# Kernel optimization log

Measured on AMD Instinct MI355X. Metric: run time of the kernel, lower is better.

Reference implementation:

```python
import jax, jax.numpy as jnp
import numpy as np

B, N, D, C, S = 128, 100000, 256, 2000, 751  # batch, memory size, feat dim, num classes, source classes
TEMP = 0.05
EPS = 1e-06


def _l2norm(x):
    return x / jnp.linalg.norm(x, axis=-1, keepdims=True)


def setup_inputs() -> dict:
    key = jax.random.key(0)
    k1, k2, k3, k4, k5 = jax.random.split(key, 5)
    inputs = _l2norm(jax.random.normal(k1, (B, D), dtype=jnp.float32))
    inputs2 = _l2norm(jax.random.normal(k2, (B, D), dtype=jnp.float32))
    features = _l2norm(jax.random.normal(k3, (N, D), dtype=jnp.float32))
    labels = jax.random.randint(k4, (N,), 0, C)
    labels = labels.at[:C].set(jnp.arange(C))  # ensure labels.max()+1 == C
    indexes = jax.random.randint(k5, (B,), 0, N)
    return {"inputs": inputs, "inputs2": inputs2, "features": features,
            "labels": labels, "indexes": indexes, "source_classes": S}


def reference(inputs, inputs2, features, labels, indexes, source_classes):
    # memory-bank logits, [B, N]
    logits = (inputs @ features.T) / TEMP
    logits2 = (inputs2 @ features.T) / TEMP
    targets = labels[indexes]  # [B]

    # per-class counts and segment-mean of logits over the bank, [C, B]
    nums = jax.ops.segment_sum(jnp.ones((N,), jnp.float32), labels, num_segments=C)  # [C]
    denom = jnp.where(nums > 0, nums, 1.0)[:, None]  # [C, 1]
    sim = jax.ops.segment_sum(logits.T, labels, num_segments=C) / denom   # [C, B]
    sim2 = jax.ops.segment_sum(logits2.T, labels, num_segments=C) / denom  # [C, B]

    # MSE between class-probability maps over the first source_classes classes
    p1 = sim[:source_classes].T   # [B, S]
    p2 = sim2[:source_classes].T  # [B, S]
    diff = jax.nn.softmax(p1, axis=1) - jax.nn.softmax(p2, axis=1)
    loss_mse = jnp.sum(diff * diff) / source_classes

    # hard-positive/negative mining: per-class max of logits (0 for empty classes)
    seg_max = jax.ops.segment_max(logits.T, labels, num_segments=C)  # [C, B], -inf where empty
    present = (nums > 0)  # [C]
    sim_hard = jnp.where(present[:, None], seg_max, 0.0).T  # [B, C]
    # for the target class, use the hardest (min) positive instead
    seg_min = jax.ops.segment_min(logits.T, labels, num_segments=C)  # [C, B]
    b_idx = jnp.arange(B)
    sim_hard = sim_hard.at[b_idx, targets].set(seg_min[targets, b_idx])

    # masked softmax over present classes + NLL
    mask = present.astype(jnp.float32)[None, :]  # [1, C]
    exps = jnp.exp(sim_hard) * mask
    masked_sim = exps / (jnp.sum(exps, axis=1, keepdims=True) + EPS)
    loss_con = -jnp.mean(jnp.log(masked_sim[b_idx, targets] + EPS))

    return (loss_con, loss_mse)
```

## Files before the change

### kernel.cpp

```cpp
#include <hip/hip_runtime.h>
#include <hip/hip_bf16.h>

#define BB 128
#define NN 100000
#define DD 256
#define CC 2000
#define SS 751
#define INVTEMP 20.0f
#define EPSV 1e-6f

#define HIST_BLOCKS 391
#define PREP_BLOCKS 32
#define NTILES_MAX 3563

typedef __attribute__((ext_vector_type(8))) short bf16x8;
typedef __attribute__((ext_vector_type(8))) unsigned short u16x8;
typedef __attribute__((ext_vector_type(4))) float f32x4;

__device__ __forceinline__ unsigned short f2bf(float x) {
    unsigned int u = __float_as_uint(x);
    u += 0x7fffu + ((u >> 16) & 1u);
    return (unsigned short)(u >> 16);
}

__device__ __forceinline__ bf16x8 cvt8(float4 a, float4 b) {
    union { unsigned u[4]; bf16x8 v; } cv;
    asm("v_cvt_pk_bf16_f32 %0, %1, %2" : "=v"(cv.u[0]) : "v"(a.x), "v"(a.y));
    asm("v_cvt_pk_bf16_f32 %0, %1, %2" : "=v"(cv.u[1]) : "v"(a.z), "v"(a.w));
    asm("v_cvt_pk_bf16_f32 %0, %1, %2" : "=v"(cv.u[2]) : "v"(b.x), "v"(b.y));
    asm("v_cvt_pk_bf16_f32 %0, %1, %2" : "=v"(cv.u[3]) : "v"(b.z), "v"(b.w));
    return cv.v;
}

__global__ __launch_bounds__(256) void hist_prep_kernel(
    const int* __restrict__ labels, int* __restrict__ counts,
    const float* __restrict__ in1, const float* __restrict__ in2,
    unsigned short* __restrict__ inb)
{
    int bid = blockIdx.x;
    if (bid < HIST_BLOCKS) {
        int n = bid * 256 + threadIdx.x;
        if (n < NN) atomicAdd(&counts[labels[n]], 1);
    } else {
        int ch = (bid - HIST_BLOCKS) * 256 + threadIdx.x;
        if (ch >= 8192) return;
        int l  = ch & 63;
        int kc = (ch >> 6) & 7;
        int nr = ch >> 9;
        int row = nr * 16 + (l & 15);
        const float* src = (row < BB) ? (in1 + (size_t)row * DD)
                                      : (in2 + (size_t)(row - BB) * DD);
        int k0 = kc * 32 + ((l >> 4) << 3);
        u16x8 o;
        #pragma unroll
        for (int j = 0; j < 8; ++j) o[j] = f2bf(src[k0 + j]);
        *(u16x8*)(inb + (size_t)ch * 8) = o;
    }
}

__global__ __launch_bounds__(256) void scan_kernel(const int* __restrict__ counts,
                                                   int* __restrict__ tile_start,
                                                   int* __restrict__ cursor,
                                                   int* __restrict__ tile_meta,
                                                   int* __restrict__ ntiles_total,
                                                   float* __restrict__ out) {
    const int PT = 8;
    int tid = threadIdx.x;
    if (tid == 0) { out[0] = 0.f; out[1] = 0.f; }
    int tcnt[PT];
    int tot = 0;
    #pragma unroll
    for (int i = 0; i < PT; ++i) {
        int c = tid * PT + i;
        tcnt[i] = (c < CC) ? ((counts[c] + 63) >> 6) : 0;
        tot += tcnt[i];
    }
    __shared__ int sh[256];
    sh[tid] = tot;
    __syncthreads();
    for (int ofs = 1; ofs < 256; ofs <<= 1) {
        int v = (tid >= ofs) ? sh[tid - ofs] : 0;
        __syncthreads();
        sh[tid] += v;
        __syncthreads();
    }
    if (tid == 255) *ntiles_total = sh[255];
    int run = sh[tid] - tot;
    #pragma unroll
    for (int i = 0; i < PT; ++i) {
        int c = tid * PT + i;
        if (c < CC) {
            tile_start[c] = run;
            cursor[c] = run << 6;
            for (int j = 0; j < tcnt[i]; ++j)
                tile_meta[run + j] = (c << 5) | j;
        }
        run += tcnt[i];
    }
}

__global__ void scatter_idx(const int* __restrict__ labels, int* __restrict__ cursor,
                            int* __restrict__ sorted_idx) {
    int n = blockIdx.x * 256 + threadIdx.x;
    if (n < NN) {
        int c = labels[n];
        int p = atomicAdd(&cursor[c], 1);
        sorted_idx[p] = n;
    }
}

__global__ __launch_bounds__(512, 4) void mm_kernel(
    const float* __restrict__ features, const unsigned short* __restrict__ inb,
    const int* __restrict__ sorted_idx, const int* __restrict__ tile_meta,
    const int* __restrict__ counts, const int* __restrict__ ntiles_total,
    float* __restrict__ part_max, float* __restrict__ part_min,
    float* __restrict__ part_sA, float* __restrict__ part_sB)
{
    const int t = blockIdx.x;
    if (t >= *ntiles_total) return;
    const int tid = threadIdx.x;
    const int w   = tid >> 6;
    const int l   = tid & 63;
    const int meta = tile_meta[t];
    const int base_local = (meta & 31) << 6;
    const int cnt  = counts[meta >> 5];
    const int vrows = cnt - base_local;

    __shared__ __align__(16) char ldsF[65536];

    #pragma unroll
    for (int i2 = 0; i2 < 8; ++i2) {
        int row = w * 8 + i2;
        int idx = t * 64 + ((row < vrows) ? row : 0);
        int n   = sorted_idx[idx];
        const float* src = features + (size_t)n * DD + ((l ^ (row & 7)) << 2);
        __builtin_amdgcn_global_load_lds(
            (const __attribute__((address_space(1))) void*)src,
            (__attribute__((address_space(3))) void*)(&ldsF[0] + (row << 10)),
            16, 0, 0);
    }
    __syncthreads();

    f32x4 acc[4][2];
    #pragma unroll
    for (int ma = 0; ma < 4; ++ma)
        #pragma unroll
        for (int nb = 0; nb < 2; ++nb)
            acc[ma][nb] = (f32x4){0.f, 0.f, 0.f, 0.f};

    const int rlow = l & 15;
    const int cbase = (l >> 4) << 1;

    bf16x8 bcur0 = *(const bf16x8*)(inb + (((size_t)((2 * w + 0) * 8 + 0) * 64 + l) << 3));
    bf16x8 bcur1 = *(const bf16x8*)(inb + (((size_t)((2 * w + 1) * 8 + 0) * 64 + l) << 3));

    __builtin_amdgcn_s_setprio(1);
    #pragma unroll
    for (int kc = 0; kc < 8; ++kc) {
        bf16x8 bnx0 = bcur0, bnx1 = bcur1;
        if (kc < 7) {
            bnx0 = *(const bf16x8*)(inb + (((size_t)((2 * w + 0) * 8 + kc + 1) * 64 + l) << 3));
            bnx1 = *(const bf16x8*)(inb + (((size_t)((2 * w + 1) * 8 + kc + 1) * 64 + l) << 3));
        }
        #pragma unroll
        for (int ma = 0; ma < 4; ++ma) {
            int r  = 16 * ma + rlow;
            int x  = r & 7;
            int c0 = kc * 8 + cbase;
            const char* Lr = &ldsF[0] + (r << 10);
            float4 f0 = *(const float4*)(Lr + (((c0    ) ^ x) << 4));
            float4 f1 = *(const float4*)(Lr + (((c0 + 1) ^ x) << 4));
            bf16x8 a = cvt8(f0, f1);
            acc[ma][0] = __builtin_amdgcn_mfma_f32_16x16x32_bf16(a, bcur0, acc[ma][0], 0, 0, 0);
            acc[ma][1] = __builtin_amdgcn_mfma_f32_16x16x32_bf16(a, bcur1, acc[ma][1], 0, 0, 0);
        }
        bcur0 = bnx0; bcur1 = bnx1;
    }
    __builtin_amdgcn_s_setprio(0);

    const int h4 = (l >> 4) << 2;
    float sm[2] = {0.f, 0.f};
    float mx[2] = {-3.4e38f, -3.4e38f};
    float mn[2] = { 3.4e38f,  3.4e38f};
    #pragma unroll
    for (int ma = 0; ma < 4; ++ma) {
        #pragma unroll
        for (int reg = 0; reg < 4; ++reg) {
            bool valid = (16 * ma + h4 + reg) < vrows;
            if (valid) {
                #pragma unroll
                for (int nb = 0; nb < 2; ++nb) {
                    float v = acc[ma][nb][reg];
                    sm[nb] += v;
                    if (w < 4) {
                        mx[nb] = fmaxf(mx[nb], v);
                        mn[nb] = fminf(mn[nb], v);
                    }
                }
            }
        }
    }
    #pragma unroll
    for (int nb = 0; nb < 2; ++nb) {
        sm[nb] += __shfl_xor(sm[nb], 16);
        sm[nb] += __shfl_xor(sm[nb], 32);
        if (w < 4) {
            mx[nb] = fmaxf(mx[nb], __shfl_xor(mx[nb], 16));
            mx[nb] = fmaxf(mx[nb], __shfl_xor(mx[nb], 32));
            mn[nb] = fminf(mn[nb], __shfl_xor(mn[nb], 16));
            mn[nb] = fminf(mn[nb], __shfl_xor(mn[nb], 32));
        }
    }
    if (l < 16) {
        #pragma unroll
        for (int nb = 0; nb < 2; ++nb) {
            int col = 32 * (w & 3) + 16 * nb + l;
            size_t p = (size_t)t * 128 + col;
            if (w < 4) { part_max[p] = mx[nb]; part_min[p] = mn[nb]; part_sA[p] = sm[nb]; }
            else       { part_sB[p] = sm[nb]; }
        }
    }
}


__device__ __forceinline__ float blk_reduce_sum(float v) {
    __shared__ float sh[4];
    int lane = threadIdx.x & 63, w = threadIdx.x >> 6;
    #pragma unroll
    for (int o = 32; o; o >>= 1) v += __shfl_down(v, o, 64);
    __syncthreads();
    if (lane == 0) sh[w] = v;
    __syncthreads();
    return sh[0] + sh[1] + sh[2] + sh[3];
}

__device__ __forceinline__ float blk_reduce_max(float v) {
    __shared__ float sh[4];
    int lane = threadIdx.x & 63, w = threadIdx.x >> 6;
    #pragma unroll
    for (int o = 32; o; o >>= 1) v = fmaxf(v, __shfl_down(v, o, 64));
    __syncthreads();
    if (lane == 0) sh[w] = v;
    __syncthreads();
    return fmaxf(fmaxf(sh[0], sh[1]), fmaxf(sh[2], sh[3]));
}

__global__ __launch_bounds__(256) void finalize_kernel(
    const float* __restrict__ part_max, const float* __restrict__ part_min,
    const float* __restrict__ part_sA, const float* __restrict__ part_sB,
    const int* __restrict__ tile_start, const int* __restrict__ counts,
    const int* __restrict__ labels, const int* __restrict__ indexes,
    float* __restrict__ out)
{
    const int b   = blockIdx.x;
    const int tid = threadIdx.x;
    const int tgt = labels[indexes[b]];

    __shared__ float a1[SS], a2[SS];
    __shared__ float sh_etgt;

    float local = 0.f;
    for (int c = tid; c < CC; c += 256) {
        int cnt = counts[c];
        if (cnt > 0) {
            int t0 = tile_start[c];
            int nt = (cnt + 63) >> 6;
            bool src = (c < SS);
            float mx = -3.4e38f, sA = 0.f, sB = 0.f;
            for (int j = 0; j < nt; ++j) {
                size_t p = (size_t)(t0 + j) * 128 + b;
                mx = fmaxf(mx, part_max[p]);
                if (src) { sA += part_sA[p]; sB += part_sB[p]; }
            }
            float v = mx;
            if (c == tgt) {
                float mn = 3.4e38f;
                for (int j = 0; j < nt; ++j)
                    mn = fminf(mn, part_min[(size_t)(t0 + j) * 128 + b]);
                v = mn;
            }
            float e = expf(v * INVTEMP);
            local += e;
            if (c == tgt) sh_etgt = e;
            if (src) {
                float icnt = INVTEMP / (float)cnt;
                a1[c] = sA * icnt;
                a2[c] = sB * icnt;
            }
        } else if (c < SS) {
            a1[c] = 0.f;
            a2[c] = 0.f;
        }
    }
    float sum_e = blk_reduce_sum(local);
    float etgt = sh_etgt;
    float loss_con_b = -logf(etgt / (sum_e + EPSV) + EPSV);

    float m1 = -3.4e38f, m2 = -3.4e38f;
    for (int c = tid; c < SS; c += 256) { m1 = fmaxf(m1, a1[c]); m2 = fmaxf(m2, a2[c]); }
    m1 = blk_reduce_max(m1);
    m2 = blk_reduce_max(m2);
    float s1 = 0.f, s2 = 0.f;
    for (int c = tid; c < SS; c += 256) { s1 += expf(a1[c] - m1); s2 += expf(a2[c] - m2); }
    s1 = blk_reduce_sum(s1);
    s2 = blk_reduce_sum(s2);
    float inv1 = 1.f / s1, inv2 = 1.f / s2;
    float dsum = 0.f;
    for (int c = tid; c < SS; c += 256) {
        float d = expf(a1[c] - m1) * inv1 - expf(a2[c] - m2) * inv2;
        dsum += d * d;
    }
    dsum = blk_reduce_sum(dsum);
    if (tid == 0) {
        atomicAdd(&out[0], loss_con_b * (1.0f / (float)BB));
        atomicAdd(&out[1], dsum * (1.0f / (float)SS));
    }
}


extern "C" void kernel_launch(void* const* d_in, const int* in_sizes, int n_in,
                              void* d_out, int out_size, void* d_ws, size_t ws_size,
                              hipStream_t stream) {
    const float* inputs   = (const float*)d_in[0];
    const float* inputs2  = (const float*)d_in[1];
    const float* features = (const float*)d_in[2];
    const int*   labels   = (const int*)d_in[3];
    const int*   indexes  = (const int*)d_in[4];

    float* out = (float*)d_out;

    int* wsi = (int*)d_ws;
    int* counts     = wsi;
    int* tile_start = wsi + 2048;
    int* cursor     = wsi + 4096;
    int* ntiles     = wsi + 6144;
    unsigned short* inb = (unsigned short*)(wsi + 6160);
    int* tile_meta  = wsi + 38928;
    int* sorted_idx = wsi + 42496;
    float* part_max = (float*)(wsi + 270592);
    float* part_min = part_max + (size_t)NTILES_MAX * 128;
    float* part_sA  = part_min + (size_t)NTILES_MAX * 128;
    float* part_sB  = part_sA  + (size_t)NTILES_MAX * 128;

    hipMemsetAsync(counts, 0, 2048 * sizeof(int), stream);

    hist_prep_kernel<<<HIST_BLOCKS + PREP_BLOCKS, 256, 0, stream>>>(
        labels, counts, inputs, inputs2, inb);
    scan_kernel<<<1, 256, 0, stream>>>(counts, tile_start, cursor, tile_meta, ntiles, out);
    scatter_idx<<<HIST_BLOCKS, 256, 0, stream>>>(labels, cursor, sorted_idx);
    mm_kernel<<<NTILES_MAX, 512, 0, stream>>>(features, inb, sorted_idx, tile_meta,
                                              counts, ntiles,
                                              part_max, part_min, part_sA, part_sB);
    finalize_kernel<<<BB, 256, 0, stream>>>(part_max, part_min, part_sA, part_sB,
                                            tile_start, counts, labels, indexes, out);
}
```

Measured before the change: 98.91 us.

## Convert feature tile to bf16 once when staging into LDS

The feature tile is no longer copied into LDS as fp32 with async global_load_lds and then converted to bf16 by each of the 8 waves. Each thread now loads fp32 rows through registers, converts them to bf16 once, and writes them to a swizzled MFMA-ready LDS layout. This halves LDS use (32KB) and removes the redundant per-wave conversions and LDS reads. In exchange it loses the asynchronous direct-to-LDS load path, and the prefetch of the B operand across the k loop is dropped.

```diff
diff --git a/kernel.cpp b/kernel.cpp
--- a/kernel.cpp
+++ b/kernel.cpp
@@ -23,8 +23,8 @@
     return (unsigned short)(u >> 16);
 }
 
-__device__ __forceinline__ bf16x8 cvt8(float4 a, float4 b) {
-    union { unsigned u[4]; bf16x8 v; } cv;
+__device__ __forceinline__ u16x8 cvt8u(float4 a, float4 b) {
+    union { unsigned u[4]; u16x8 v; } cv;
     asm("v_cvt_pk_bf16_f32 %0, %1, %2" : "=v"(cv.u[0]) : "v"(a.x), "v"(a.y));
     asm("v_cvt_pk_bf16_f32 %0, %1, %2" : "=v"(cv.u[1]) : "v"(a.z), "v"(a.w));
     asm("v_cvt_pk_bf16_f32 %0, %1, %2" : "=v"(cv.u[2]) : "v"(b.x), "v"(b.y));
@@ -126,18 +126,27 @@
     const int cnt  = counts[meta >> 5];
     const int vrows = cnt - base_local;
 
-    __shared__ __align__(16) char ldsF[65536];
-
-    #pragma unroll
-    for (int i2 = 0; i2 < 8; ++i2) {
-        int row = w * 8 + i2;
-        int idx = t * 64 + ((row < vrows) ? row : 0);
+    __shared__ __align__(16) char ldsA[32768];
+
+    {
+        const int m0 = tid >> 3;
+        const int g  = tid & 7;
+        int idx = t * 64 + ((m0 < vrows) ? m0 : 0);
         int n   = sorted_idx[idx];
-        const float* src = features + (size_t)n * DD + ((l ^ (row & 7)) << 2);
-        __builtin_amdgcn_global_load_lds(
-            (const __attribute__((address_space(1))) void*)src,
-            (__attribute__((address_space(3))) void*)(&ldsF[0] + (row << 10)),
-            16, 0, 0);
+        const float* src = features + (size_t)n * DD;
+        const int ma = m0 >> 4;
+        #pragma unroll
+        for (int s = 0; s < 4; ++s) {
+            int k0 = s * 64 + g * 8;
+            float4 a = *(const float4*)(src + k0);
+            float4 b = *(const float4*)(src + k0 + 4);
+            u16x8 o = cvt8u(a, b);
+            int crow = s * 8 + g;
+            int kc   = crow >> 2;
+            int ks   = crow & 3;
+            int cch  = (ks << 4) | ((m0 & 15) ^ kc);
+            *(u16x8*)(&ldsA[0] + (((ma * 8 + kc) << 10) | (cch << 4))) = o;
+        }
     }
     __syncthreads();
 
@@ -148,33 +157,18 @@
         for (int nb = 0; nb < 2; ++nb)
             acc[ma][nb] = (f32x4){0.f, 0.f, 0.f, 0.f};
 
-    const int rlow = l & 15;
-    const int cbase = (l >> 4) << 1;
-
-    bf16x8 bcur0 = *(const bf16x8*)(inb + (((size_t)((2 * w + 0) * 8 + 0) * 64 + l) << 3));
-    bf16x8 bcur1 = *(const bf16x8*)(inb + (((size_t)((2 * w + 1) * 8 + 0) * 64 + l) << 3));
-
     __builtin_amdgcn_s_setprio(1);
     #pragma unroll
     for (int kc = 0; kc < 8; ++kc) {
-        bf16x8 bnx0 = bcur0, bnx1 = bcur1;
-        if (kc < 7) {
-            bnx0 = *(const bf16x8*)(inb + (((size_t)((2 * w + 0) * 8 + kc + 1) * 64 + l) << 3));
-            bnx1 = *(const bf16x8*)(inb + (((size_t)((2 * w + 1) * 8 + kc + 1) * 64 + l) << 3));
-        }
+        bf16x8 b0 = *(const bf16x8*)(inb + (((size_t)((2 * w + 0) * 8 + kc) * 64 + l) << 3));
+        bf16x8 b1 = *(const bf16x8*)(inb + (((size_t)((2 * w + 1) * 8 + kc) * 64 + l) << 3));
+        int lx = (l ^ kc) << 4;
         #pragma unroll
         for (int ma = 0; ma < 4; ++ma) {
-            int r  = 16 * ma + rlow;
-            int x  = r & 7;
-            int c0 = kc * 8 + cbase;
-            const char* Lr = &ldsF[0] + (r << 10);
-            float4 f0 = *(const float4*)(Lr + (((c0    ) ^ x) << 4));
-            float4 f1 = *(const float4*)(Lr + (((c0 + 1) ^ x) << 4));
-            bf16x8 a = cvt8(f0, f1);
-            acc[ma][0] = __builtin_amdgcn_mfma_f32_16x16x32_bf16(a, bcur0, acc[ma][0], 0, 0, 0);
-            acc[ma][1] = __builtin_amdgcn_mfma_f32_16x16x32_bf16(a, bcur1, acc[ma][1], 0, 0, 0);
-        }
-        bcur0 = bnx0; bcur1 = bnx1;
+            bf16x8 a = *(const bf16x8*)(&ldsA[0] + ((ma * 8 + kc) << 10) + lx);
+            acc[ma][0] = __builtin_amdgcn_mfma_f32_16x16x32_bf16(a, b0, acc[ma][0], 0, 0, 0);
+            acc[ma][1] = __builtin_amdgcn_mfma_f32_16x16x32_bf16(a, b1, acc[ma][1], 0, 0, 0);
+        }
     }
     __builtin_amdgcn_s_setprio(0);
 
```

New measurement: 93.43 us. 1.06x faster.
